# Performance work log

Hardware: AMD Instinct MI355X
Metric: run time of the kernel (lower is better)

## Reference

```python
import jax, jax.numpy as jnp
import numpy as np

NH, NKV, HD = 32, 8, 64      # query heads, kv heads, head dim
H, INTER = 2048, 8192        # hidden, mlp intermediate
B, NBLK, BS = 32, 256, 16    # batch, blocks per seq, block size
NUM_BLOCKS = B * NBLK
EPS = 1e-5
THETA = 10000.0


def rms_norm(x, w):
    var = jnp.mean(x * x, axis=-1, keepdims=True)
    return x * jax.lax.rsqrt(var + EPS) * w


def rotate_half(x):
    x1, x2 = jnp.split(x, 2, axis=-1)
    return jnp.concatenate([-x2, x1], axis=-1)


def setup_inputs() -> dict:
    key = jax.random.key(0)
    ks = jax.random.split(key, 12)
    s = 0.02
    x = jax.random.normal(ks[0], (B, 1, H), jnp.float32)
    k_cache = jax.random.normal(ks[1], (NUM_BLOCKS, BS, NKV, HD), jnp.float32)
    v_cache = jax.random.normal(ks[2], (NUM_BLOCKS, BS, NKV, HD), jnp.float32)
    block_table = jnp.arange(B * NBLK, dtype=jnp.int32).reshape(B, NBLK)
    cache_seqlens = jax.random.randint(ks[3], (B,), 0, NBLK * BS - 1, jnp.int32)
    return {
        'x': x, 'k_cache': k_cache, 'v_cache': v_cache,
        'ln1_w': jnp.ones((H,), jnp.float32),
        'q_w': jax.random.normal(ks[4], (H, NH * HD), jnp.float32) * s,
        'k_w': jax.random.normal(ks[5], (H, NKV * HD), jnp.float32) * s,
        'v_w': jax.random.normal(ks[6], (H, NKV * HD), jnp.float32) * s,
        'o_w': jax.random.normal(ks[7], (NH * HD, H), jnp.float32) * s,
        'ln2_w': jnp.ones((H,), jnp.float32),
        'gate_w': jax.random.normal(ks[8], (H, INTER), jnp.float32) * s,
        'up_w': jax.random.normal(ks[9], (H, INTER), jnp.float32) * s,
        'down_w': jax.random.normal(ks[10], (INTER, H), jnp.float32) * s,
        'block_table': block_table,
        'cache_seqlens': cache_seqlens,
        'block_size': BS,
    }


def reference(x, k_cache, v_cache, ln1_w, q_w, k_w, v_w, o_w, ln2_w,
              gate_w, up_w, down_w, block_table, cache_seqlens, block_size):
    b = x.shape[0]
    normed = rms_norm(x, ln1_w)[:, 0, :]                     # [B,H]
    q = (normed @ q_w).reshape(b, NH, HD)                    # [B,NH,HD]
    k = (normed @ k_w).reshape(b, NKV, HD)                   # [B,NKV,HD]
    v = (normed @ v_w).reshape(b, NKV, HD)

    # RoPE at current position (HF rotate_half convention)
    pos = cache_seqlens.astype(jnp.float32)                  # [B]
    inv_freq = 1.0 / (THETA ** (jnp.arange(0, HD, 2, dtype=jnp.float32) / HD))
    ang = pos[:, None] * inv_freq[None, :]                   # [B,HD/2]
    cos = jnp.concatenate([jnp.cos(ang), jnp.cos(ang)], -1)[:, None, :]  # [B,1,HD]
    sin = jnp.concatenate([jnp.sin(ang), jnp.sin(ang)], -1)[:, None, :]
    q = q * cos + rotate_half(q) * sin
    k = k * cos + rotate_half(k) * sin

    # paged cache update: write new k/v at block_table[b, pos//bs], offset pos%bs
    blk = block_table[jnp.arange(b), cache_seqlens // block_size]
    flat_idx = blk.astype(jnp.int32) * block_size + cache_seqlens % block_size  # [B]
    kc = k_cache.reshape(-1, NKV, HD).at[flat_idx].set(k).reshape(k_cache.shape)
    vc = v_cache.reshape(-1, NKV, HD).at[flat_idx].set(v).reshape(v_cache.shape)

    # gather paged KV via block table -> [B, S, NKV, HD]
    K = kc[block_table].reshape(b, -1, NKV, HD)
    V = vc[block_table].reshape(b, -1, NKV, HD)
    S = K.shape[1]

    # decode attention with GQA: head h uses kv head h // (NH//NKV)
    G = NH // NKV
    qh = q.reshape(b, NKV, G, HD)
    scores = jnp.einsum('bkgd,bskd->bkgs', qh, K) / jnp.sqrt(jnp.float32(HD))
    valid = (jnp.arange(S)[None, :] <= cache_seqlens[:, None])  # seqlen+1 tokens
    scores = jnp.where(valid[:, None, None, :], scores, -jnp.inf)
    probs = jax.nn.softmax(scores, axis=-1)
    attn = jnp.einsum('bkgs,bskd->bkgd', probs, V).reshape(b, NH * HD)

    x = x + (attn @ o_w)[:, None, :]

    h = rms_norm(x, ln2_w)
    mlp = (jax.nn.silu(h @ gate_w) * (h @ up_w)) @ down_w
    return x + mlp
```

## Files before the change

kernel.cpp:

```cpp
#include <hip/hip_runtime.h>
#include <math.h>

#define B_      32
#define H_      2048
#define NH_     32
#define NKV_    8
#define HD_     64
#define G_      4
#define INTER_  8192
#define NBLK_   256
#define BS_     16
#define NCHUNK_ 8
#define CHUNK_  512

#define OFF_NORMED_T  0
#define OFF_QKV       65536
#define OFF_QROPE     163840
#define OFF_X2        229376
#define OFF_HT        294912
#define OFF_ATTN_T    360448
#define OFF_G         425984
#define OFF_U         688128
#define OFF_ACT_T     950272
#define OFF_OPART     1212416
#define OFF_MPART     1736704
#define OFF_LPART     1744896

__global__ __launch_bounds__(256) void init_kernel(const float* __restrict__ x,
                                                   float* __restrict__ x2,
                                                   float* __restrict__ qkv,
                                                   float* __restrict__ gu) {
    int idx = blockIdx.x * 256 + threadIdx.x;
    if (idx < 65536) x2[idx] = x[idx];
    int i2 = idx - 65536;
    if (i2 >= 0 && i2 < 98304) qkv[i2] = 0.f;
    int i3 = idx - 163840;
    if (i3 >= 0 && i3 < 524288) gu[i3] = 0.f;
}

__global__ __launch_bounds__(256) void rmsnorm_kernel(const float* __restrict__ xin,
                                                      const float* __restrict__ w,
                                                      float* __restrict__ out_t,
                                                      float* __restrict__ copyout) {
    int b = blockIdx.x, tid = threadIdx.x;
    const float* xr = xin + (size_t)b * H_;
    float xv[8];
    float ss = 0.f;
#pragma unroll
    for (int j = 0; j < 8; ++j) {
        xv[j] = xr[tid + j * 256];
        ss += xv[j] * xv[j];
    }
#pragma unroll
    for (int off = 32; off >= 1; off >>= 1) ss += __shfl_xor(ss, off, 64);
    __shared__ float red[4];
    __shared__ float rbc;
    if ((tid & 63) == 0) red[tid >> 6] = ss;
    __syncthreads();
    if (tid == 0) rbc = rsqrtf((red[0] + red[1] + red[2] + red[3]) / (float)H_ + 1e-5f);
    __syncthreads();
    float r = rbc;
#pragma unroll
    for (int j = 0; j < 8; ++j) {
        int i = tid + j * 256;
        out_t[(size_t)i * B_ + b] = xv[j] * r * w[i];
        if (copyout) copyout[(size_t)b * H_ + i] = xv[j];
    }
}

__device__ __forceinline__ void gemv_block(const float* __restrict__ xt,
                                           const float* __restrict__ W, int Nw,
                                           int wcolbase, int krange,
                                           float* __restrict__ out, int Nout,
                                           int outcolbase, bool atomic_out) {
    int tid = threadIdx.x;
    int ct  = tid & 63;
    int ks  = __builtin_amdgcn_readfirstlane(tid >> 6);
    int rows = krange >> 2;
    int kb0 = blockIdx.y * krange + ks * rows;
    int wcol = wcolbase + ct;

    float acc[B_];
#pragma unroll
    for (int b = 0; b < B_; ++b) acc[b] = 0.f;

    const float* Wp  = W + (size_t)kb0 * Nw + wcol;
    const float* xp0 = xt + (size_t)kb0 * B_;
#pragma unroll 4
    for (int k = 0; k < rows; ++k) {
        float wv = Wp[(size_t)k * Nw];
        const float* xp = xp0 + k * B_;
#pragma unroll
        for (int b = 0; b < B_; ++b) acc[b] = fmaf(xp[b], wv, acc[b]);
    }

    __shared__ float red[2080];
#pragma unroll
    for (int b0 = 0; b0 < B_; b0 += 8) {
#pragma unroll
        for (int bb = 0; bb < 8; ++bb) red[(ks * 8 + bb) * 65 + ct] = acc[b0 + bb];
        __syncthreads();
        for (int p = tid; p < 512; p += 256) {
            int bb = p >> 6, c2 = p & 63;
            float s = red[bb * 65 + c2] + red[(8 + bb) * 65 + c2] +
                      red[(16 + bb) * 65 + c2] + red[(24 + bb) * 65 + c2];
            float* op = out + (size_t)(b0 + bb) * Nout + outcolbase + c2;
            if (atomic_out) atomicAdd(op, s); else *op = s;
        }
        __syncthreads();
    }
}

__global__ __launch_bounds__(256) void gemv_qkv_kernel(const float* __restrict__ xt,
                                                       const float* __restrict__ qw,
                                                       const float* __restrict__ kw,
                                                       const float* __restrict__ vw,
                                                       float* __restrict__ qkv) {
    int cb = blockIdx.x;
    const float* W; int Nw, wbase;
    if (cb < 32)      { W = qw; Nw = 2048; wbase = cb << 6; }
    else if (cb < 40) { W = kw; Nw = 512;  wbase = (cb - 32) << 6; }
    else              { W = vw; Nw = 512;  wbase = (cb - 40) << 6; }
    gemv_block(xt, W, Nw, wbase, 512, qkv, 3072, cb << 6, true);
}

__global__ __launch_bounds__(256) void gemv_o_kernel(const float* __restrict__ xt,
                                                     const float* __restrict__ W,
                                                     float* __restrict__ x2) {
    gemv_block(xt, W, 2048, blockIdx.x << 6, 256, x2, 2048, blockIdx.x << 6, true);
}

__global__ __launch_bounds__(256) void gemv_gateup_kernel(const float* __restrict__ xt,
                                                          const float* __restrict__ gw,
                                                          const float* __restrict__ uw,
                                                          float* __restrict__ g,
                                                          float* __restrict__ u) {
    int cb = blockIdx.x;
    const float* W; float* out; int wbase;
    if (cb < 128) { W = gw; out = g; wbase = cb << 6; }
    else          { W = uw; out = u; wbase = (cb - 128) << 6; }
    gemv_block(xt, W, 8192, wbase, 1024, out, 8192, wbase, true);
}

__global__ __launch_bounds__(256) void gemv_down_kernel(const float* __restrict__ xt,
                                                        const float* __restrict__ W,
                                                        float* __restrict__ dout) {
    gemv_block(xt, W, 2048, blockIdx.x << 6, 1024, dout, 2048, blockIdx.x << 6, true);
}

__global__ __launch_bounds__(256) void rope_cache_kernel(const float* __restrict__ qkv,
                                                         const int* __restrict__ btab,
                                                         const int* __restrict__ seqlens,
                                                         float* __restrict__ qrope,
                                                         float* __restrict__ kc,
                                                         float* __restrict__ vc) {
    int b = blockIdx.x, tid = threadIdx.x;
    int pos = seqlens[b];
    const float* qkvb = qkv + (size_t)b * 3072;
    const float LOG2T = 13.287712379549449f;
    float fpos = (float)pos;
#pragma unroll
    for (int j = 0; j < 8; ++j) {
        int i = tid + j * 256;
        int d = i & 63, ii = d & 31;
        float ang = fpos * exp2f(-(float)(2 * ii) * (LOG2T / 64.f));
        float c = cosf(ang), s = sinf(ang);
        float v1 = qkvb[i];
        float v2 = qkvb[(d < 32) ? i + 32 : i - 32];
        qrope[(size_t)b * 2048 + i] = (d < 32) ? (v1 * c - v2 * s) : (v1 * c + v2 * s);
    }
    int blk = btab[b * NBLK_ + (pos >> 4)];
    size_t cbase = (size_t)(blk * BS_ + (pos & 15)) * NKV_ * HD_;
    for (int i = tid; i < NKV_ * HD_; i += 256) {
        int d = i & 63, ii = d & 31;
        float ang = fpos * exp2f(-(float)(2 * ii) * (LOG2T / 64.f));
        float c = cosf(ang), s = sinf(ang);
        float v1 = qkvb[2048 + i];
        float v2 = qkvb[2048 + ((d < 32) ? i + 32 : i - 32)];
        kc[cbase + i] = (d < 32) ? (v1 * c - v2 * s) : (v1 * c + v2 * s);
        vc[cbase + i] = qkvb[2560 + i];
    }
}

__global__ __launch_bounds__(256) void attn_chunk_kernel(const float* __restrict__ qrope,
                                                         const float* __restrict__ kc,
                                                         const float* __restrict__ vc,
                                                         const int* __restrict__ btab,
                                                         const int* __restrict__ seqlens,
                                                         float* __restrict__ opart,
                                                         float* __restrict__ mpart,
                                                         float* __restrict__ lpart) {
    int cx = blockIdx.x, kv = blockIdx.y, b = blockIdx.z;
    int tid = threadIdx.x;
    int pos = seqlens[b];
    int c0 = cx * CHUNK_;
    int pidx = ((b * NKV_ + kv) * NCHUNK_ + cx) * G_;
    if (c0 > pos) {
        if (tid < G_) { mpart[pidx + tid] = -__builtin_inff(); lpart[pidx + tid] = 0.f; }
        return;
    }
    __shared__ float qlds[G_][HD_];
    __shared__ float slds[G_][CHUNK_];
    {
        int h = tid >> 6, d = tid & 63;
        qlds[h][d] = qrope[((size_t)b * NH_ + kv * G_ + h) * HD_ + d] * 0.125f;
    }
    __syncthreads();

    int grp = tid >> 4, ln = tid & 15;
    const int* bt = btab + b * NBLK_;
    for (int tb = 0; tb < CHUNK_; tb += 16) {
        int tl = tb + grp;
        int t = c0 + tl;
        int blk = bt[t >> 4];
        const float4 k4 = *(const float4*)(kc + ((size_t)(blk * BS_ + (t & 15)) * NKV_ + kv) * HD_ + ln * 4);
        bool valid = (t <= pos);
#pragma unroll
        for (int h = 0; h < G_; ++h) {
            const float4 q4 = *(const float4*)&qlds[h][ln * 4];
            float p = q4.x * k4.x + q4.y * k4.y + q4.z * k4.z + q4.w * k4.w;
#pragma unroll
            for (int off = 8; off >= 1; off >>= 1) p += __shfl_xor(p, off, 16);
            if (ln == 0) slds[h][tl] = valid ? p : -__builtin_inff();
        }
    }
    __syncthreads();

    int h = tid >> 6, lane = tid & 63;
    float m = -__builtin_inff();
    for (int i = lane; i < CHUNK_; i += 64) m = fmaxf(m, slds[h][i]);
#pragma unroll
    for (int off = 32; off >= 1; off >>= 1) m = fmaxf(m, __shfl_xor(m, off, 64));
    float l = 0.f;
    for (int i = lane; i < CHUNK_; i += 64) {
        float p = expf(slds[h][i] - m);
        slds[h][i] = p;
        l += p;
    }
#pragma unroll
    for (int off = 32; off >= 1; off >>= 1) l += __shfl_xor(l, off, 64);
    if (lane == 0) { mpart[pidx + h] = m; lpart[pidx + h] = l; }
    __syncthreads();

    int d = lane;
    float o = 0.f;
    int tmax = min(CHUNK_, pos + 1 - c0);
    for (int tl = 0; tl < tmax; ++tl) {
        int t = c0 + tl;
        int blk = bt[t >> 4];
        o = fmaf(slds[h][tl], vc[((size_t)(blk * BS_ + (t & 15)) * NKV_ + kv) * HD_ + d], o);
    }
    opart[(size_t)(pidx + h) * HD_ + d] = o;
}

__global__ __launch_bounds__(64) void attn_reduce_kernel(const float* __restrict__ opart,
                                                         const float* __restrict__ mpart,
                                                         const float* __restrict__ lpart,
                                                         float* __restrict__ attn_t) {
    int hq = blockIdx.x, b = blockIdx.y;
    int kv = hq >> 2, g = hq & 3;
    int lane = threadIdx.x;
    int base = ((b * NKV_ + kv) * NCHUNK_) * G_ + g;
    float mv[NCHUNK_], lv[NCHUNK_];
    float M = -__builtin_inff();
#pragma unroll
    for (int c = 0; c < NCHUNK_; ++c) {
        mv[c] = mpart[base + c * G_];
        lv[c] = lpart[base + c * G_];
        M = fmaxf(M, mv[c]);
    }
    float L = 0.f, o = 0.f;
#pragma unroll
    for (int c = 0; c < NCHUNK_; ++c) {
        if (lv[c] > 0.f) {
            float f = expf(mv[c] - M);
            L += lv[c] * f;
            o += f * opart[(size_t)(base + c * G_) * HD_ + lane];
        }
    }
    attn_t[(size_t)(hq * HD_ + lane) * B_ + b] = o / L;
}

__global__ __launch_bounds__(256) void silu_mul_kernel(const float* __restrict__ g,
                                                       const float* __restrict__ u,
                                                       float* __restrict__ act_t) {
    __shared__ float tile[8][33];
    int j0 = blockIdx.x * 8;
    int tid = threadIdx.x;
    int jj = tid & 7, b = tid >> 3;
    float gv = g[(size_t)b * INTER_ + j0 + jj];
    float uv = u[(size_t)b * INTER_ + j0 + jj];
    tile[jj][b] = (gv / (1.f + expf(-gv))) * uv;
    __syncthreads();
    int b2 = tid & 31, j2 = tid >> 5;
    act_t[(size_t)(j0 + j2) * B_ + b2] = tile[j2][b2];
}

extern "C" void kernel_launch(void* const* d_in, const int* in_sizes, int n_in,
                              void* d_out, int out_size, void* d_ws, size_t ws_size,
                              hipStream_t stream) {
    const float* x       = (const float*)d_in[0];
    float*       k_cache = (float*)d_in[1];
    float*       v_cache = (float*)d_in[2];
    const float* ln1_w   = (const float*)d_in[3];
    const float* q_w     = (const float*)d_in[4];
    const float* k_w     = (const float*)d_in[5];
    const float* v_w     = (const float*)d_in[6];
    const float* o_w     = (const float*)d_in[7];
    const float* ln2_w   = (const float*)d_in[8];
    const float* gate_w  = (const float*)d_in[9];
    const float* up_w    = (const float*)d_in[10];
    const float* down_w  = (const float*)d_in[11];
    const int*   btab    = (const int*)d_in[12];
    const int*   seql    = (const int*)d_in[13];
    float* out = (float*)d_out;

    float* ws = (float*)d_ws;
    float* normed_t = ws + OFF_NORMED_T;
    float* qkv      = ws + OFF_QKV;
    float* qrope    = ws + OFF_QROPE;
    float* x2       = ws + OFF_X2;
    float* ht       = ws + OFF_HT;
    float* attn_t   = ws + OFF_ATTN_T;
    float* gbuf     = ws + OFF_G;
    float* ubuf     = ws + OFF_U;
    float* act_t    = ws + OFF_ACT_T;
    float* opart    = ws + OFF_OPART;
    float* mpart    = ws + OFF_MPART;
    float* lpart    = ws + OFF_LPART;

    init_kernel<<<2688, 256, 0, stream>>>(x, x2, qkv, gbuf );
    rmsnorm_kernel<<<32, 256, 0, stream>>>(x, ln1_w, normed_t, nullptr);
    gemv_qkv_kernel<<<dim3(48, 4), 256, 0, stream>>>(normed_t, q_w, k_w, v_w, qkv);
    rope_cache_kernel<<<32, 256, 0, stream>>>(qkv, btab, seql, qrope, k_cache, v_cache);
    attn_chunk_kernel<<<dim3(NCHUNK_, NKV_, B_), 256, 0, stream>>>(qrope, k_cache, v_cache,
                                                                   btab, seql, opart, mpart, lpart);
    attn_reduce_kernel<<<dim3(NH_, B_), 64, 0, stream>>>(opart, mpart, lpart, attn_t);
    gemv_o_kernel<<<dim3(32, 8), 256, 0, stream>>>(attn_t, o_w, x2);
    rmsnorm_kernel<<<32, 256, 0, stream>>>(x2, ln2_w, ht, out);
    gemv_gateup_kernel<<<dim3(256, 2), 256, 0, stream>>>(ht, gate_w, up_w, gbuf, ubuf);
    silu_mul_kernel<<<1024, 256, 0, stream>>>(gbuf, ubuf, act_t);
    gemv_down_kernel<<<dim3(32, 8), 256, 0, stream>>>(act_t, down_w, out);
}
```

Before: 799.5 us.

## Replace atomic GEMV split-K with float4 partial buffers and fused reduce kernels

Each GEMV now has every lane compute four adjacent columns using float4 weight loads. Split-K partial sums are written to workspace buffers instead of being atomically added into zero-initialized outputs. The reductions are folded into the following kernels: RoPE plus cache write, residual plus second RMSNorm, and SiLU-mul, plus a separate reduce for the down projection. This removes the init kernel. Attention now caches block-table entries in LDS and stages V tiles through shared memory for coalesced loads. The cost is more registers per thread (a 128-float accumulator), larger workspace traffic for the partials, and extra reduce passes.

```diff
diff --git a/kernel.cpp b/kernel.cpp
--- a/kernel.cpp
+++ b/kernel.cpp
@@ -13,35 +13,22 @@
 #define NCHUNK_ 8
 #define CHUNK_  512
 
-#define OFF_NORMED_T  0
-#define OFF_QKV       65536
-#define OFF_QROPE     163840
-#define OFF_X2        229376
-#define OFF_HT        294912
-#define OFF_ATTN_T    360448
-#define OFF_G         425984
-#define OFF_U         688128
-#define OFF_ACT_T     950272
-#define OFF_OPART     1212416
-#define OFF_MPART     1736704
-#define OFF_LPART     1744896
-
-__global__ __launch_bounds__(256) void init_kernel(const float* __restrict__ x,
-                                                   float* __restrict__ x2,
-                                                   float* __restrict__ qkv,
-                                                   float* __restrict__ gu) {
-    int idx = blockIdx.x * 256 + threadIdx.x;
-    if (idx < 65536) x2[idx] = x[idx];
-    int i2 = idx - 65536;
-    if (i2 >= 0 && i2 < 98304) qkv[i2] = 0.f;
-    int i3 = idx - 163840;
-    if (i3 >= 0 && i3 < 524288) gu[i3] = 0.f;
-}
+#define OFF_NORMED_T 0
+#define OFF_QKV_P    65536
+#define OFF_QROPE    1638400
+#define OFF_HT       1703936
+#define OFF_ATTN_T   1769472
+#define OFF_GU_P     1835008
+#define OFF_ACT_T    6029312
+#define OFF_O_P      6291456
+#define OFF_D_P      7340032
+#define OFF_OPART    9437184
+#define OFF_MPART    9961472
+#define OFF_LPART    9969664
 
 __global__ __launch_bounds__(256) void rmsnorm_kernel(const float* __restrict__ xin,
                                                       const float* __restrict__ w,
-                                                      float* __restrict__ out_t,
-                                                      float* __restrict__ copyout) {
+                                                      float* __restrict__ out_t) {
     int b = blockIdx.x, tid = threadIdx.x;
     const float* xr = xin + (size_t)b * H_;
     float xv[8];
@@ -64,132 +51,141 @@
     for (int j = 0; j < 8; ++j) {
         int i = tid + j * 256;
         out_t[(size_t)i * B_ + b] = xv[j] * r * w[i];
-        if (copyout) copyout[(size_t)b * H_ + i] = xv[j];
-    }
-}
-
-__device__ __forceinline__ void gemv_block(const float* __restrict__ xt,
-                                           const float* __restrict__ W, int Nw,
-                                           int wcolbase, int krange,
-                                           float* __restrict__ out, int Nout,
-                                           int outcolbase, bool atomic_out) {
+    }
+}
+
+__device__ __forceinline__ void gemv4_block(const float* __restrict__ xt,
+                                            const float* __restrict__ W, int Nw,
+                                            int wcol0, int rowsPerWave,
+                                            float* __restrict__ part, int Nout,
+                                            int outcol0) {
     int tid = threadIdx.x;
-    int ct  = tid & 63;
-    int ks  = __builtin_amdgcn_readfirstlane(tid >> 6);
-    int rows = krange >> 2;
-    int kb0 = blockIdx.y * krange + ks * rows;
-    int wcol = wcolbase + ct;
-
-    float acc[B_];
-#pragma unroll
-    for (int b = 0; b < B_; ++b) acc[b] = 0.f;
-
-    const float* Wp  = W + (size_t)kb0 * Nw + wcol;
-    const float* xp0 = xt + (size_t)kb0 * B_;
-#pragma unroll 4
-    for (int k = 0; k < rows; ++k) {
-        float wv = Wp[(size_t)k * Nw];
-        const float* xp = xp0 + k * B_;
-#pragma unroll
-        for (int b = 0; b < B_; ++b) acc[b] = fmaf(xp[b], wv, acc[b]);
-    }
-
-    __shared__ float red[2080];
-#pragma unroll
-    for (int b0 = 0; b0 < B_; b0 += 8) {
-#pragma unroll
-        for (int bb = 0; bb < 8; ++bb) red[(ks * 8 + bb) * 65 + ct] = acc[b0 + bb];
+    int lane = tid & 63;
+    int ks = tid >> 6;
+    int k0 = (blockIdx.y * 4 + ks) * rowsPerWave;
+    int wcol = wcol0 + lane * 4;
+
+    float acc[4][B_];
+#pragma unroll
+    for (int c = 0; c < 4; ++c)
+#pragma unroll
+        for (int b = 0; b < B_; ++b) acc[c][b] = 0.f;
+
+    const float* Wp = W + (size_t)k0 * Nw + wcol;
+    const float* xp = xt + (size_t)k0 * B_;
+#pragma unroll 2
+    for (int k = 0; k < rowsPerWave; ++k) {
+        float4 w4 = *(const float4*)(Wp + (size_t)k * Nw);
+        const float* xr = xp + k * B_;
+#pragma unroll
+        for (int b = 0; b < B_; ++b) {
+            float xv = xr[b];
+            acc[0][b] = fmaf(w4.x, xv, acc[0][b]);
+            acc[1][b] = fmaf(w4.y, xv, acc[1][b]);
+            acc[2][b] = fmaf(w4.z, xv, acc[2][b]);
+            acc[3][b] = fmaf(w4.w, xv, acc[3][b]);
+        }
+    }
+
+    __shared__ float red[4][2][260];
+    float* prow = part + (size_t)blockIdx.y * B_ * Nout;
+    for (int b0 = 0; b0 < B_; b0 += 2) {
+#pragma unroll
+        for (int bi = 0; bi < 2; ++bi)
+#pragma unroll
+            for (int c = 0; c < 4; ++c)
+                red[ks][bi][lane * 4 + c] = acc[c][b0 + bi];
         __syncthreads();
-        for (int p = tid; p < 512; p += 256) {
-            int bb = p >> 6, c2 = p & 63;
-            float s = red[bb * 65 + c2] + red[(8 + bb) * 65 + c2] +
-                      red[(16 + bb) * 65 + c2] + red[(24 + bb) * 65 + c2];
-            float* op = out + (size_t)(b0 + bb) * Nout + outcolbase + c2;
-            if (atomic_out) atomicAdd(op, s); else *op = s;
+#pragma unroll
+        for (int bi = 0; bi < 2; ++bi) {
+            float s = red[0][bi][tid] + red[1][bi][tid] + red[2][bi][tid] + red[3][bi][tid];
+            prow[(size_t)(b0 + bi) * Nout + outcol0 + tid] = s;
         }
         __syncthreads();
     }
 }
 
-__global__ __launch_bounds__(256) void gemv_qkv_kernel(const float* __restrict__ xt,
-                                                       const float* __restrict__ qw,
-                                                       const float* __restrict__ kw,
-                                                       const float* __restrict__ vw,
-                                                       float* __restrict__ qkv) {
+__global__ __launch_bounds__(256, 2) void gemv_qkv_kernel(const float* __restrict__ xt,
+                                                          const float* __restrict__ qw,
+                                                          const float* __restrict__ kw,
+                                                          const float* __restrict__ vw,
+                                                          float* __restrict__ part) {
     int cb = blockIdx.x;
-    const float* W; int Nw, wbase;
-    if (cb < 32)      { W = qw; Nw = 2048; wbase = cb << 6; }
-    else if (cb < 40) { W = kw; Nw = 512;  wbase = (cb - 32) << 6; }
-    else              { W = vw; Nw = 512;  wbase = (cb - 40) << 6; }
-    gemv_block(xt, W, Nw, wbase, 512, qkv, 3072, cb << 6, true);
-}
-
-__global__ __launch_bounds__(256) void gemv_o_kernel(const float* __restrict__ xt,
-                                                     const float* __restrict__ W,
-                                                     float* __restrict__ x2) {
-    gemv_block(xt, W, 2048, blockIdx.x << 6, 256, x2, 2048, blockIdx.x << 6, true);
-}
-
-__global__ __launch_bounds__(256) void gemv_gateup_kernel(const float* __restrict__ xt,
-                                                          const float* __restrict__ gw,
-                                                          const float* __restrict__ uw,
-                                                          float* __restrict__ g,
-                                                          float* __restrict__ u) {
+    if (cb < 8)       gemv4_block(xt, qw, 2048, cb * 256, 32, part, 3072, cb * 256);
+    else if (cb < 10) gemv4_block(xt, kw, 512, (cb - 8) * 256, 32, part, 3072, cb * 256);
+    else              gemv4_block(xt, vw, 512, (cb - 10) * 256, 32, part, 3072, cb * 256);
+}
+
+__global__ __launch_bounds__(256, 2) void gemv_o_kernel(const float* __restrict__ xt,
+                                                        const float* __restrict__ W,
+                                                        float* __restrict__ part) {
+    gemv4_block(xt, W, 2048, blockIdx.x * 256, 32, part, 2048, blockIdx.x * 256);
+}
+
+__global__ __launch_bounds__(256, 2) void gemv_gateup_kernel(const float* __restrict__ xt,
+                                                             const float* __restrict__ gw,
+                                                             const float* __restrict__ uw,
+                                                             float* __restrict__ part) {
     int cb = blockIdx.x;
-    const float* W; float* out; int wbase;
-    if (cb < 128) { W = gw; out = g; wbase = cb << 6; }
-    else          { W = uw; out = u; wbase = (cb - 128) << 6; }
-    gemv_block(xt, W, 8192, wbase, 1024, out, 8192, wbase, true);
-}
-
-__global__ __launch_bounds__(256) void gemv_down_kernel(const float* __restrict__ xt,
-                                                        const float* __restrict__ W,
-                                                        float* __restrict__ dout) {
-    gemv_block(xt, W, 2048, blockIdx.x << 6, 1024, dout, 2048, blockIdx.x << 6, true);
-}
-
-__global__ __launch_bounds__(256) void rope_cache_kernel(const float* __restrict__ qkv,
-                                                         const int* __restrict__ btab,
-                                                         const int* __restrict__ seqlens,
-                                                         float* __restrict__ qrope,
-                                                         float* __restrict__ kc,
-                                                         float* __restrict__ vc) {
+    if (cb < 32) gemv4_block(xt, gw, 8192, cb * 256, 64, part, 16384, cb * 256);
+    else         gemv4_block(xt, uw, 8192, (cb - 32) * 256, 64, part, 16384, 8192 + (cb - 32) * 256);
+}
+
+__global__ __launch_bounds__(256, 2) void gemv_down_kernel(const float* __restrict__ xt,
+                                                           const float* __restrict__ W,
+                                                           float* __restrict__ part) {
+    gemv4_block(xt, W, 2048, blockIdx.x * 256, 64, part, 2048, blockIdx.x * 256);
+}
+
+__global__ __launch_bounds__(256) void qkv_reduce_rope_kernel(const float* __restrict__ part,
+                                                              const int* __restrict__ btab,
+                                                              const int* __restrict__ seql,
+                                                              float* __restrict__ qrope,
+                                                              float* __restrict__ kc,
+                                                              float* __restrict__ vc) {
     int b = blockIdx.x, tid = threadIdx.x;
-    int pos = seqlens[b];
-    const float* qkvb = qkv + (size_t)b * 3072;
+    __shared__ float s[3072];
+#pragma unroll
+    for (int j = 0; j < 12; ++j) {
+        int col = tid + j * 256;
+        float a = 0.f;
+#pragma unroll
+        for (int y = 0; y < 16; ++y) a += part[((size_t)y * B_ + b) * 3072 + col];
+        s[col] = a;
+    }
+    __syncthreads();
+    int pos = seql[b];
+    float fpos = (float)pos;
     const float LOG2T = 13.287712379549449f;
-    float fpos = (float)pos;
 #pragma unroll
     for (int j = 0; j < 8; ++j) {
         int i = tid + j * 256;
         int d = i & 63, ii = d & 31;
         float ang = fpos * exp2f(-(float)(2 * ii) * (LOG2T / 64.f));
-        float c = cosf(ang), s = sinf(ang);
-        float v1 = qkvb[i];
-        float v2 = qkvb[(d < 32) ? i + 32 : i - 32];
-        qrope[(size_t)b * 2048 + i] = (d < 32) ? (v1 * c - v2 * s) : (v1 * c + v2 * s);
+        float c = cosf(ang), sn = sinf(ang);
+        float v1 = s[i], v2 = s[(d < 32) ? i + 32 : i - 32];
+        qrope[(size_t)b * 2048 + i] = (d < 32) ? (v1 * c - v2 * sn) : (v1 * c + v2 * sn);
     }
     int blk = btab[b * NBLK_ + (pos >> 4)];
     size_t cbase = (size_t)(blk * BS_ + (pos & 15)) * NKV_ * HD_;
     for (int i = tid; i < NKV_ * HD_; i += 256) {
         int d = i & 63, ii = d & 31;
         float ang = fpos * exp2f(-(float)(2 * ii) * (LOG2T / 64.f));
-        float c = cosf(ang), s = sinf(ang);
-        float v1 = qkvb[2048 + i];
-        float v2 = qkvb[2048 + ((d < 32) ? i + 32 : i - 32)];
-        kc[cbase + i] = (d < 32) ? (v1 * c - v2 * s) : (v1 * c + v2 * s);
-        vc[cbase + i] = qkvb[2560 + i];
-    }
-}
-
-__global__ __launch_bounds__(256) void attn_chunk_kernel(const float* __restrict__ qrope,
-                                                         const float* __restrict__ kc,
-                                                         const float* __restrict__ vc,
-                                                         const int* __restrict__ btab,
-                                                         const int* __restrict__ seqlens,
-                                                         float* __restrict__ opart,
-                                                         float* __restrict__ mpart,
-                                                         float* __restrict__ lpart) {
+        float c = cosf(ang), sn = sinf(ang);
+        float v1 = s[2048 + i], v2 = s[2048 + ((d < 32) ? i + 32 : i - 32)];
+        kc[cbase + i] = (d < 32) ? (v1 * c - v2 * sn) : (v1 * c + v2 * sn);
+        vc[cbase + i] = s[2560 + i];
+    }
+}
+
+__global__ __launch_bounds__(256, 4) void attn_chunk_kernel(const float* __restrict__ qrope,
+                                                            const float* __restrict__ kc,
+                                                            const float* __restrict__ vc,
+                                                            const int* __restrict__ btab,
+                                                            const int* __restrict__ seqlens,
+                                                            float* __restrict__ opart,
+                                                            float* __restrict__ mpart,
+                                                            float* __restrict__ lpart) {
     int cx = blockIdx.x, kv = blockIdx.y, b = blockIdx.z;
     int tid = threadIdx.x;
     int pos = seqlens[b];
@@ -201,6 +197,9 @@
     }
     __shared__ float qlds[G_][HD_];
     __shared__ float slds[G_][CHUNK_];
+    __shared__ float vt[32][HD_];
+    __shared__ int btl[32];
+    if (tid < 32) btl[tid] = btab[b * NBLK_ + (c0 >> 4) + tid];
     {
         int h = tid >> 6, d = tid & 63;
         qlds[h][d] = qrope[((size_t)b * NH_ + kv * G_ + h) * HD_ + d] * 0.125f;
@@ -208,11 +207,10 @@
     __syncthreads();
 
     int grp = tid >> 4, ln = tid & 15;
-    const int* bt = btab + b * NBLK_;
     for (int tb = 0; tb < CHUNK_; tb += 16) {
         int tl = tb + grp;
         int t = c0 + tl;
-        int blk = bt[t >> 4];
+        int blk = btl[tl >> 4];
         const float4 k4 = *(const float4*)(kc + ((size_t)(blk * BS_ + (t & 15)) * NKV_ + kv) * HD_ + ln * 4);
         bool valid = (t <= pos);
 #pragma unroll
@@ -245,10 +243,20 @@
     int d = lane;
     float o = 0.f;
     int tmax = min(CHUNK_, pos + 1 - c0);
-    for (int tl = 0; tl < tmax; ++tl) {
-        int t = c0 + tl;
-        int blk = bt[t >> 4];
-        o = fmaf(slds[h][tl], vc[((size_t)(blk * BS_ + (t & 15)) * NKV_ + kv) * HD_ + d], o);
+    for (int t0 = 0; t0 < tmax; t0 += 32) {
+#pragma unroll
+        for (int r = 0; r < 2; ++r) {
+            int tl = t0 + r * 16 + (tid >> 4);
+            int t = c0 + tl;
+            int blk = btl[tl >> 4];
+            *(float4*)&vt[r * 16 + (tid >> 4)][(tid & 15) * 4] =
+                *(const float4*)(vc + ((size_t)(blk * BS_ + (t & 15)) * NKV_ + kv) * HD_ + (tid & 15) * 4);
+        }
+        __syncthreads();
+#pragma unroll 8
+        for (int tl2 = 0; tl2 < 32; ++tl2)
+            o = fmaf(slds[h][t0 + tl2], vt[tl2][d], o);
+        __syncthreads();
     }
     opart[(size_t)(pidx + h) * HD_ + d] = o;
 }
@@ -281,19 +289,73 @@
     attn_t[(size_t)(hq * HD_ + lane) * B_ + b] = o / L;
 }
 
-__global__ __launch_bounds__(256) void silu_mul_kernel(const float* __restrict__ g,
-                                                       const float* __restrict__ u,
-                                                       float* __restrict__ act_t) {
-    __shared__ float tile[8][33];
-    int j0 = blockIdx.x * 8;
-    int tid = threadIdx.x;
-    int jj = tid & 7, b = tid >> 3;
-    float gv = g[(size_t)b * INTER_ + j0 + jj];
-    float uv = u[(size_t)b * INTER_ + j0 + jj];
-    tile[jj][b] = (gv / (1.f + expf(-gv))) * uv;
-    __syncthreads();
-    int b2 = tid & 31, j2 = tid >> 5;
-    act_t[(size_t)(j0 + j2) * B_ + b2] = tile[j2][b2];
+__global__ __launch_bounds__(256) void o_reduce_rms2_kernel(const float* __restrict__ part,
+                                                            const float* __restrict__ x,
+                                                            const float* __restrict__ w2,
+                                                            float* __restrict__ out,
+                                                            float* __restrict__ ht) {
+    int b = blockIdx.x, tid = threadIdx.x;
+    float v[8];
+    float ss = 0.f;
+#pragma unroll
+    for (int j = 0; j < 8; ++j) {
+        int col = tid + j * 256;
+        float a = x[(size_t)b * H_ + col];
+#pragma unroll
+        for (int y = 0; y < 16; ++y) a += part[((size_t)y * B_ + b) * 2048 + col];
+        v[j] = a;
+        ss += a * a;
+    }
+#pragma unroll
+    for (int off = 32; off >= 1; off >>= 1) ss += __shfl_xor(ss, off, 64);
+    __shared__ float red[4];
+    __shared__ float rbc;
+    if ((tid & 63) == 0) red[tid >> 6] = ss;
+    __syncthreads();
+    if (tid == 0) rbc = rsqrtf((red[0] + red[1] + red[2] + red[3]) / (float)H_ + 1e-5f);
+    __syncthreads();
+    float r = rbc;
+#pragma unroll
+    for (int j = 0; j < 8; ++j) {
+        int col = tid + j * 256;
+        out[(size_t)b * H_ + col] = v[j];
+        ht[(size_t)col * B_ + b] = v[j] * r * w2[col];
+    }
+}
+
+__global__ __launch_bounds__(256) void gu_reduce_silu_kernel(const float* __restrict__ part,
+                                                             float* __restrict__ act_t) {
+    int j0 = blockIdx.x * 64, tid = threadIdx.x;
+    int jj = tid & 63, bq = tid >> 6;
+    __shared__ float tile[64][33];
+#pragma unroll
+    for (int bb = 0; bb < 8; ++bb) {
+        int b = bq * 8 + bb;
+        float g = 0.f, u = 0.f;
+#pragma unroll
+        for (int y = 0; y < 8; ++y) {
+            size_t base = ((size_t)y * B_ + b) * 16384 + j0 + jj;
+            g += part[base];
+            u += part[base + 8192];
+        }
+        tile[jj][b] = (g / (1.f + expf(-g))) * u;
+    }
+    __syncthreads();
+#pragma unroll
+    for (int r = 0; r < 8; ++r) {
+        int j = r * 8 + (tid >> 5);
+        int bc = tid & 31;
+        act_t[(size_t)(j0 + j) * B_ + bc] = tile[j][bc];
+    }
+}
+
+__global__ __launch_bounds__(256) void down_reduce_kernel(const float* __restrict__ part,
+                                                          float* __restrict__ out) {
+    int idx = blockIdx.x * 256 + threadIdx.x;
+    float a = out[idx];
+#pragma unroll
+    for (int y = 0; y < 32; ++y) a += part[(size_t)y * 65536 + idx];
+    out[idx] = a;
 }
 
 extern "C" void kernel_launch(void* const* d_in, const int* in_sizes, int n_in,
@@ -317,28 +379,28 @@
 
     float* ws = (float*)d_ws;
     float* normed_t = ws + OFF_NORMED_T;
-    float* qkv      = ws + OFF_QKV;
+    float* qkv_p    = ws + OFF_QKV_P;
     float* qrope    = ws + OFF_QROPE;
-    float* x2       = ws + OFF_X2;
     float* ht       = ws + OFF_HT;
     float* attn_t   = ws + OFF_ATTN_T;
-    float* gbuf     = ws + OFF_G;
-    float* ubuf     = ws + OFF_U;
+    float* gu_p     = ws + OFF_GU_P;
     float* act_t    = ws + OFF_ACT_T;
+    float* o_p      = ws + OFF_O_P;
+    float* d_p      = ws + OFF_D_P;
     float* opart    = ws + OFF_OPART;
     float* mpart    = ws + OFF_MPART;
     float* lpart    = ws + OFF_LPART;
 
-    init_kernel<<<2688, 256, 0, stream>>>(x, x2, qkv, gbuf );
-    rmsnorm_kernel<<<32, 256, 0, stream>>>(x, ln1_w, normed_t, nullptr);
-    gemv_qkv_kernel<<<dim3(48, 4), 256, 0, stream>>>(normed_t, q_w, k_w, v_w, qkv);
-    rope_cache_kernel<<<32, 256, 0, stream>>>(qkv, btab, seql, qrope, k_cache, v_cache);
+    rmsnorm_kernel<<<32, 256, 0, stream>>>(x, ln1_w, normed_t);
+    gemv_qkv_kernel<<<dim3(12, 16), 256, 0, stream>>>(normed_t, q_w, k_w, v_w, qkv_p);
+    qkv_reduce_rope_kernel<<<32, 256, 0, stream>>>(qkv_p, btab, seql, qrope, k_cache, v_cache);
     attn_chunk_kernel<<<dim3(NCHUNK_, NKV_, B_), 256, 0, stream>>>(qrope, k_cache, v_cache,
                                                                    btab, seql, opart, mpart, lpart);
     attn_reduce_kernel<<<dim3(NH_, B_), 64, 0, stream>>>(opart, mpart, lpart, attn_t);
-    gemv_o_kernel<<<dim3(32, 8), 256, 0, stream>>>(attn_t, o_w, x2);
-    rmsnorm_kernel<<<32, 256, 0, stream>>>(x2, ln2_w, ht, out);
-    gemv_gateup_kernel<<<dim3(256, 2), 256, 0, stream>>>(ht, gate_w, up_w, gbuf, ubuf);
-    silu_mul_kernel<<<1024, 256, 0, stream>>>(gbuf, ubuf, act_t);
-    gemv_down_kernel<<<dim3(32, 8), 256, 0, stream>>>(act_t, down_w, out);
-}
+    gemv_o_kernel<<<dim3(8, 16), 256, 0, stream>>>(attn_t, o_w, o_p);
+    o_reduce_rms2_kernel<<<32, 256, 0, stream>>>(o_p, x, ln2_w, out, ht);
+    gemv_gateup_kernel<<<dim3(64, 8), 256, 0, stream>>>(ht, gate_w, up_w, gu_p);
+    gu_reduce_silu_kernel<<<128, 256, 0, stream>>>(gu_p, act_t);
+    gemv_down_kernel<<<dim3(8, 32), 256, 0, stream>>>(act_t, down_w, d_p);
+    down_reduce_kernel<<<256, 256, 0, stream>>>(d_p, out);
+}
```

After: 779.9 us. -2.4%, faster.
